# Kernel optimization log

Hardware: AMD Instinct MI355X
Metric: run time of the kernel (lower is better)

The kernel has to match this reference:

```python
import jax, jax.numpy as jnp
import numpy as np
import math

B, L, N, DIM, H = 2, 8, 1024, 512, 8
DH = DIM // H

def setup_inputs() -> dict:
    key = jax.random.key(0)
    ks = jax.random.split(key, 9)
    s = 1.0 / math.sqrt(DIM)
    return {
        "x": jax.random.normal(ks[0], (B, L, N, DIM), dtype=jnp.float32),
        "Wq": jax.random.normal(ks[1], (DIM, DIM), dtype=jnp.float32) * s,
        "bq": jnp.zeros((DIM,), dtype=jnp.float32),
        "Wk": jax.random.normal(ks[2], (DIM, DIM), dtype=jnp.float32) * s,
        "bk": jnp.zeros((DIM,), dtype=jnp.float32),
        "Wv": jax.random.normal(ks[3], (DIM, DIM), dtype=jnp.float32) * s,
        "bv": jnp.zeros((DIM,), dtype=jnp.float32),
        "Wo": jax.random.normal(ks[4], (DIM, DIM), dtype=jnp.float32) * s,
        "bo": jnp.zeros((DIM,), dtype=jnp.float32),
    }

def _split_heads(t):
    # 'b l n (h d) -> b l h n d'
    b, l, n, _ = t.shape
    return t.reshape(b, l, n, H, DH).transpose(0, 1, 3, 2, 4)

def reference(x, Wq, bq, Wk, bk, Wv, bv, Wo, bo):
    q = _split_heads(x @ Wq.T + bq)
    # FAITHFUL BUG: source maps (q, v, k) -> (q_mat, k_mat, v_mat),
    # so the "keys" come from the v projection and "values" from the k projection.
    k_mat = _split_heads(x @ Wv.T + bv)
    v_mat = _split_heads(x @ Wk.T + bk)
    # scale is sqrt(Dh * num_heads) = sqrt(dim), as in the source
    scores = jnp.einsum('blhnd,blhmd->blhnm', q, k_mat) / math.sqrt(DIM)
    weights = jax.nn.softmax(scores, axis=-1)
    inter = jnp.einsum('blhnm,blhmd->blhnd', weights, v_mat)
    # 'b l h n d -> b l n (h d)'
    inter = inter.transpose(0, 1, 3, 2, 4).reshape(x.shape[0], x.shape[1], x.shape[2], DIM)
    return inter @ Wo.T + bo
```

## Files before the change

### kernel.cpp

```cpp
#include <hip/hip_runtime.h>
#include <stdint.h>

#define DIMC 512
#define NSEQ 1024
#define BLT  16
#define NHEAD 8
#define DHD  64
#define MTOT (BLT*NSEQ)
#define LDSW 72
#define PLW  68

typedef float f32x4 __attribute__((ext_vector_type(4)));
typedef short s16x8 __attribute__((ext_vector_type(8)));

__device__ __forceinline__ unsigned short f2bf(float f) {
    unsigned int u = __float_as_uint(f);
    u += 0x7fffu + ((u >> 16) & 1u);
    return (unsigned short)(u >> 16);
}
__device__ __forceinline__ float bf2f(unsigned short h) {
    return __uint_as_float(((unsigned int)h) << 16);
}

#define QSCALE (0.04419417382415922f * 1.4426950408889634f)

__device__ __forceinline__ void gll16(const void* g, void* l) {
    __builtin_amdgcn_global_load_lds(
        (const __attribute__((address_space(1))) void*)g,
        (__attribute__((address_space(3))) void*)l, 16, 0, 0);
}

__global__ void detect_kernel(const unsigned short* __restrict__ x,
                              int* __restrict__ flag) {
    int t = threadIdx.x;
    unsigned short v = x[2 * t];
    int e = (v >> 7) & 0xFF;
    int crazy = (e < 100 || e > 137) ? 1 : 0;
    unsigned long long ball = __ballot(crazy);
    if (t == 0) flag[0] = (__popcll(ball) >= 16) ? 0 : 1;
}

struct ConvArgs {
    const void* src[9];
    unsigned short* dst[9];
};

__global__ __launch_bounds__(256) void conv_kernel(ConvArgs a, const int* __restrict__ flagp) {
    const bool isbf = (*flagp != 0);
    int b = blockIdx.x;
    int seg, idx;
    if (b < 4096)      { seg = 0; idx = (b * 256 + threadIdx.x) * 8; }
    else if (b < 4608) { int t = b - 4096; seg = 1 + (t >> 7);
                         idx = (((t & 127) * 256) + threadIdx.x) * 8; }
    else               { int i = threadIdx.x * 8; seg = 5 + (i >> 9); idx = i & 511; }
    const void* s = a.src[seg];
    unsigned short* d = a.dst[seg];
    if (isbf) {
        *(uint4*)(d + idx) = *(const uint4*)((const unsigned short*)s + idx);
    } else {
        float4 t0 = *(const float4*)((const float*)s + idx);
        float4 t1 = *(const float4*)((const float*)s + idx + 4);
        ushort4 v0{f2bf(t0.x), f2bf(t0.y), f2bf(t0.z), f2bf(t0.w)};
        ushort4 v1{f2bf(t1.x), f2bf(t1.y), f2bf(t1.z), f2bf(t1.w)};
        *(ushort4*)(d + idx)     = v0;
        *(ushort4*)(d + idx + 4) = v1;
    }
}

__device__ __forceinline__ void gemm_core_async(
    const unsigned short* __restrict__ Ap, const unsigned short* __restrict__ Wp,
    int mBase, int nBase, unsigned short* Al, unsigned short* Bl, f32x4 acc[4][4])
{
    const int wave = threadIdx.x >> 6;
    const int lane = threadIdx.x & 63;
    const int lr = lane & 15, lg = lane >> 4;
    const int wm = wave >> 1, wn = wave & 1;
    const int srow = lane >> 3;
    const int scol = (lane & 7) * 8;

    #pragma unroll
    for (int a = 0; a < 4; ++a)
        #pragma unroll
        for (int b = 0; b < 4; ++b) acc[a][b] = (f32x4){0.f, 0.f, 0.f, 0.f};

    for (int k0 = 0; k0 < DIMC; k0 += 64) {
        #pragma unroll
        for (int i = 0; i < 4; ++i) {
            int rbase = (wave * 4 + i) * 8;
            gll16(Ap + (long)(mBase + rbase + srow) * DIMC + k0 + scol, Al + rbase * 64);
            gll16(Wp + (long)(nBase + rbase + srow) * DIMC + k0 + scol, Bl + rbase * 64);
        }
        __syncthreads();

        #pragma unroll
        for (int kk = 0; kk < 64; kk += 32) {
            s16x8 af[4], bf_[4];
            #pragma unroll
            for (int a = 0; a < 4; ++a)
                af[a] = *(const s16x8*)&Al[(wm * 64 + a * 16 + lr) * 64 + kk + lg * 8];
            #pragma unroll
            for (int b = 0; b < 4; ++b)
                bf_[b] = *(const s16x8*)&Bl[(wn * 64 + b * 16 + lr) * 64 + kk + lg * 8];
            #pragma unroll
            for (int a = 0; a < 4; ++a)
                #pragma unroll
                for (int b = 0; b < 4; ++b)
                    acc[a][b] = __builtin_amdgcn_mfma_f32_16x16x32_bf16(af[a], bf_[b], acc[a][b], 0, 0, 0);
        }
        __syncthreads();
    }
}

__global__ __launch_bounds__(256) void proj_kernel(
    const unsigned short* __restrict__ xb,
    const unsigned short* __restrict__ Wqb, const unsigned short* __restrict__ Wkb,
    const unsigned short* __restrict__ Wvb,
    const unsigned short* __restrict__ bqb, const unsigned short* __restrict__ bkb,
    const unsigned short* __restrict__ bvb,
    unsigned short* __restrict__ Q, unsigned short* __restrict__ K,
    unsigned short* __restrict__ Vt)
{
    const int z = blockIdx.z;
    const unsigned short* Wp = (z == 0) ? Wqb : ((z == 1) ? Wvb : Wkb);
    const unsigned short* bp = (z == 0) ? bqb : ((z == 1) ? bvb : bkb);
    unsigned short* outp = (z == 0) ? Q : ((z == 1) ? K : Vt);
    const float oscale = (z == 0) ? QSCALE : 1.0f;

    const int mBase = blockIdx.x * 128;
    const int nBase = blockIdx.y * 128;
    const int lane = threadIdx.x & 63;
    const int lr = lane & 15, lg = lane >> 4;
    const int wm = (threadIdx.x >> 6) >> 1, wn = (threadIdx.x >> 6) & 1;

    __shared__ unsigned short Al[128 * 64];
    __shared__ unsigned short Bl[128 * 64];
    f32x4 acc[4][4];
    gemm_core_async(xb, Wp, mBase, nBase, Al, Bl, acc);

    #pragma unroll
    for (int b = 0; b < 4; ++b) {
        int j = nBase + wn * 64 + b * 16 + lr;
        float bb = bf2f(bp[j]);
        int h = j >> 6, d = j & 63;
        #pragma unroll
        for (int a = 0; a < 4; ++a) {
            int m0 = mBase + wm * 64 + a * 16 + lg * 4;
            int bl = m0 >> 10, n0 = m0 & 1023;
            if (z == 2) {
                ushort4 pk;
                unsigned short* p = (unsigned short*)&pk;
                #pragma unroll
                for (int r = 0; r < 4; ++r) p[r] = f2bf(acc[a][b][r] + bb);
                *(ushort4*)&outp[(((bl << 3) + h) << 16) + (d << 10) + n0] = pk;
            } else {
                #pragma unroll
                for (int r = 0; r < 4; ++r) {
                    float v = (acc[a][b][r] + bb) * oscale;
                    outp[(((bl << 3) + h) << 16) + ((n0 + r) << 6) + d] = f2bf(v);
                }
            }
        }
    }
}

__global__ __launch_bounds__(256) void out_gemm_kernel(
    const unsigned short* __restrict__ inter, const unsigned short* __restrict__ Wob,
    const unsigned short* __restrict__ bob, void* __restrict__ outp,
    const int* __restrict__ flagp)
{
    const bool isbf = (*flagp != 0);
    const int mBase = blockIdx.x * 128;
    const int nBase = blockIdx.y * 128;
    const int lane = threadIdx.x & 63;
    const int lr = lane & 15, lg = lane >> 4;
    const int wm = (threadIdx.x >> 6) >> 1, wn = (threadIdx.x >> 6) & 1;

    __shared__ unsigned short Al[128 * 64];
    __shared__ unsigned short Bl[128 * 64];
    f32x4 acc[4][4];
    gemm_core_async(inter, Wob, mBase, nBase, Al, Bl, acc);

    #pragma unroll
    for (int b = 0; b < 4; ++b) {
        int j = nBase + wn * 64 + b * 16 + lr;
        float bb = bf2f(bob[j]);
        #pragma unroll
        for (int a = 0; a < 4; ++a) {
            #pragma unroll
            for (int r = 0; r < 4; ++r) {
                long m = mBase + wm * 64 + a * 16 + lg * 4 + r;
                float v = acc[a][b][r] + bb;
                if (isbf) ((unsigned short*)outp)[m * DIMC + j] = f2bf(v);
                else      ((float*)outp)[m * DIMC + j] = v;
            }
        }
    }
}

__global__ __launch_bounds__(256) void attn_kernel(
    const unsigned short* __restrict__ Q, const unsigned short* __restrict__ K,
    const unsigned short* __restrict__ Vt, unsigned short* __restrict__ inter)
{
    const int inst = blockIdx.x;
    const int bh = inst >> 4;
    const int qt = inst & 15;
    const int wave = threadIdx.x >> 6;
    const int lane = threadIdx.x & 63;
    const int lr = lane & 15;
    const int lg = lane >> 4;

    const unsigned short* Qb = Q + (long)bh * (NSEQ * DHD);
    const int qrow = qt * 64 + wave * 16 + lr;
    s16x8 qf0 = *(const s16x8*)&Qb[qrow * DHD + lg * 8];
    s16x8 qf1 = *(const s16x8*)&Qb[qrow * DHD + 32 + lg * 8];

    __shared__ unsigned short Kl[64 * LDSW];
    __shared__ unsigned short Vl[64 * LDSW];
    __shared__ unsigned short Pl[4][16 * PLW];

    f32x4 o[4];
    #pragma unroll
    for (int c = 0; c < 4; ++c) o[c] = (f32x4){0.f, 0.f, 0.f, 0.f};
    float l_part[4] = {0.f, 0.f, 0.f, 0.f};

    for (int kt = 0; kt < 16; ++kt) {
        const unsigned short* Kb = K + (long)bh * (NSEQ * DHD) + kt * 64 * DHD;
        const unsigned short* Vb = Vt + (long)bh * (NSEQ * DHD) + kt * 64;

        #pragma unroll
        for (int i = 0; i < 2; ++i) {
            int f = threadIdx.x + 256 * i;
            int row = f >> 3, c8 = (f & 7) * 8;
            *(uint4*)&Kl[row * LDSW + c8] = *(const uint4*)&Kb[row * DHD + c8];
            *(uint4*)&Vl[row * LDSW + c8] = *(const uint4*)&Vb[row * NSEQ + c8];
        }
        __syncthreads();

        f32x4 s[4];
        #pragma unroll
        for (int c = 0; c < 4; ++c) s[c] = (f32x4){0.f, 0.f, 0.f, 0.f};
        #pragma unroll
        for (int kk = 0; kk < 2; ++kk) {
            s16x8 a = kk ? qf1 : qf0;
            #pragma unroll
            for (int c = 0; c < 4; ++c) {
                s16x8 b = *(const s16x8*)&Kl[(c * 16 + lr) * LDSW + kk * 32 + lg * 8];
                s[c] = __builtin_amdgcn_mfma_f32_16x16x32_bf16(a, b, s[c], 0, 0, 0);
            }
        }

        #pragma unroll
        for (int c = 0; c < 4; ++c)
            #pragma unroll
            for (int r = 0; r < 4; ++r) {
                float p = __builtin_exp2f(s[c][r]);
                l_part[r] += p;
                Pl[wave][(lg * 4 + r) * PLW + c * 16 + lr] = f2bf(p);
            }

        #pragma unroll
        for (int kk = 0; kk < 2; ++kk) {
            s16x8 a = *(const s16x8*)&Pl[wave][lr * PLW + kk * 32 + lg * 8];
            #pragma unroll
            for (int c = 0; c < 4; ++c) {
                s16x8 b = *(const s16x8*)&Vl[(c * 16 + lr) * LDSW + kk * 32 + lg * 8];
                o[c] = __builtin_amdgcn_mfma_f32_16x16x32_bf16(a, b, o[c], 0, 0, 0);
            }
        }
        __syncthreads();
    }

    #pragma unroll
    for (int r = 0; r < 4; ++r) {
        #pragma unroll
        for (int msk = 1; msk < 16; msk <<= 1)
            l_part[r] += __shfl_xor(l_part[r], msk);
    }
    const int bl = bh >> 3, h = bh & 7;
    #pragma unroll
    for (int r = 0; r < 4; ++r) {
        float inv = 1.f / l_part[r];
        int n = qt * 64 + wave * 16 + lg * 4 + r;
        #pragma unroll
        for (int c = 0; c < 4; ++c) {
            int col = h * 64 + c * 16 + lr;
            inter[((long)(bl * NSEQ + n)) * DIMC + col] = f2bf(o[c][r] * inv);
        }
    }
}

extern "C" void kernel_launch(void* const* d_in, const int* in_sizes, int n_in,
                              void* d_out, int out_size, void* d_ws, size_t ws_size,
                              hipStream_t stream) {
    const void* x  = d_in[0];
    const void* Wq = d_in[1]; const void* bq = d_in[2];
    const void* Wk = d_in[3]; const void* bk = d_in[4];
    const void* Wv = d_in[5]; const void* bv = d_in[6];
    const void* Wo = d_in[7]; const void* bo = d_in[8];

    char* ws = (char*)d_ws;
    int* flag = (int*)ws;
    unsigned short* xb  = (unsigned short*)(ws + 256);
    unsigned short* Q   = xb + (long)MTOT * DIMC;
    unsigned short* K   = Q  + (long)MTOT * DIMC;
    unsigned short* Vt  = K  + (long)MTOT * DIMC;
    unsigned short* Wqb = Vt + (long)MTOT * DIMC;
    unsigned short* Wkb = Wqb + DIMC * DIMC;
    unsigned short* Wvb = Wkb + DIMC * DIMC;
    unsigned short* Wob = Wvb + DIMC * DIMC;
    unsigned short* bqb = Wob + DIMC * DIMC;
    unsigned short* bkb = bqb + DIMC;
    unsigned short* bvb = bkb + DIMC;
    unsigned short* bob = bvb + DIMC;

    detect_kernel<<<1, 64, 0, stream>>>((const unsigned short*)x, flag);

    ConvArgs ca;
    ca.src[0] = x;  ca.src[1] = Wq; ca.src[2] = Wk; ca.src[3] = Wv; ca.src[4] = Wo;
    ca.src[5] = bq; ca.src[6] = bk; ca.src[7] = bv; ca.src[8] = bo;
    ca.dst[0] = xb;  ca.dst[1] = Wqb; ca.dst[2] = Wkb; ca.dst[3] = Wvb; ca.dst[4] = Wob;
    ca.dst[5] = bqb; ca.dst[6] = bkb; ca.dst[7] = bvb; ca.dst[8] = bob;
    conv_kernel<<<4609, 256, 0, stream>>>(ca, flag);

    dim3 gp(MTOT / 128, DIMC / 128, 3);
    proj_kernel<<<gp, 256, 0, stream>>>(xb, Wqb, Wkb, Wvb, bqb, bkb, bvb, Q, K, Vt);

    attn_kernel<<<BLT * NHEAD * 16, 256, 0, stream>>>(Q, K, Vt, xb );

    dim3 go(MTOT / 128, DIMC / 128);
    out_gemm_kernel<<<go, 256, 0, stream>>>(xb , Wob, bob, d_out, flag);
}
```

Measured before the change: 252.9 us.

## Keep attention probabilities in registers via transposed MFMA and swizzle LDS

Measured after the change: 248.4 us. No clear change (-1.8%).

```diff
diff --git a/kernel.cpp b/kernel.cpp
--- a/kernel.cpp
+++ b/kernel.cpp
@@ -7,11 +7,10 @@
 #define NHEAD 8
 #define DHD  64
 #define MTOT (BLT*NSEQ)
-#define LDSW 72
-#define PLW  68
 
 typedef float f32x4 __attribute__((ext_vector_type(4)));
 typedef short s16x8 __attribute__((ext_vector_type(8)));
+typedef short s16x4 __attribute__((ext_vector_type(4)));
 
 __device__ __forceinline__ unsigned short f2bf(float f) {
     unsigned int u = __float_as_uint(f);
@@ -30,14 +29,22 @@
         (__attribute__((address_space(3))) void*)l, 16, 0, 0);
 }
 
-__global__ void detect_kernel(const unsigned short* __restrict__ x,
-                              int* __restrict__ flag) {
-    int t = threadIdx.x;
+__device__ __forceinline__ f32x4 mfma16_bf16(s16x4 a, s16x4 b, f32x4 c) {
+#if __has_builtin(__builtin_amdgcn_mfma_f32_16x16x16bf16_1k)
+    return __builtin_amdgcn_mfma_f32_16x16x16bf16_1k(a, b, c, 0, 0, 0);
+#else
+    asm volatile("v_mfma_f32_16x16x16_bf16 %0, %1, %2, %0"
+                 : "+v"(c) : "v"(a), "v"(b));
+    return c;
+#endif
+}
+
+__device__ __forceinline__ bool detect_bf16(const unsigned short* x) {
+    int t = threadIdx.x & 63;
     unsigned short v = x[2 * t];
     int e = (v >> 7) & 0xFF;
-    int crazy = (e < 100 || e > 137) ? 1 : 0;
-    unsigned long long ball = __ballot(crazy);
-    if (t == 0) flag[0] = (__popcll(ball) >= 16) ? 0 : 1;
+    unsigned long long ball = __ballot(e < 100 || e > 137);
+    return __popcll(ball) < 16;
 }
 
 struct ConvArgs {
@@ -45,8 +52,9 @@
     unsigned short* dst[9];
 };
 
-__global__ __launch_bounds__(256) void conv_kernel(ConvArgs a, const int* __restrict__ flagp) {
-    const bool isbf = (*flagp != 0);
+__global__ __launch_bounds__(256) void conv_kernel(ConvArgs a,
+                                                   const unsigned short* __restrict__ xdet) {
+    const bool isbf = detect_bf16(xdet);
     int b = blockIdx.x;
     int seg, idx;
     if (b < 4096)      { seg = 0; idx = (b * 256 + threadIdx.x) * 8; }
@@ -166,9 +174,9 @@
 __global__ __launch_bounds__(256) void out_gemm_kernel(
     const unsigned short* __restrict__ inter, const unsigned short* __restrict__ Wob,
     const unsigned short* __restrict__ bob, void* __restrict__ outp,
-    const int* __restrict__ flagp)
+    const unsigned short* __restrict__ xdet)
 {
-    const bool isbf = (*flagp != 0);
+    const bool isbf = detect_bf16(xdet);
     const int mBase = blockIdx.x * 128;
     const int nBase = blockIdx.y * 128;
     const int lane = threadIdx.x & 63;
@@ -196,6 +204,8 @@
         }
     }
 }
+
+#define SWZ(row, col) ((row) * 64 + ((col) ^ (((row) & 7) * 8)))
 
 __global__ __launch_bounds__(256) void attn_kernel(
     const unsigned short* __restrict__ Q, const unsigned short* __restrict__ K,
@@ -214,14 +224,13 @@
     s16x8 qf0 = *(const s16x8*)&Qb[qrow * DHD + lg * 8];
     s16x8 qf1 = *(const s16x8*)&Qb[qrow * DHD + 32 + lg * 8];
 
-    __shared__ unsigned short Kl[64 * LDSW];
-    __shared__ unsigned short Vl[64 * LDSW];
-    __shared__ unsigned short Pl[4][16 * PLW];
+    __shared__ unsigned short Kl[64 * 64];
+    __shared__ unsigned short Vl[64 * 64];
 
     f32x4 o[4];
     #pragma unroll
-    for (int c = 0; c < 4; ++c) o[c] = (f32x4){0.f, 0.f, 0.f, 0.f};
-    float l_part[4] = {0.f, 0.f, 0.f, 0.f};
+    for (int m = 0; m < 4; ++m) o[m] = (f32x4){0.f, 0.f, 0.f, 0.f};
+    float l_acc = 0.f;
 
     for (int kt = 0; kt < 16; ++kt) {
         const unsigned short* Kb = K + (long)bh * (NSEQ * DHD) + kt * 64 * DHD;
@@ -231,8 +240,8 @@
         for (int i = 0; i < 2; ++i) {
             int f = threadIdx.x + 256 * i;
             int row = f >> 3, c8 = (f & 7) * 8;
-            *(uint4*)&Kl[row * LDSW + c8] = *(const uint4*)&Kb[row * DHD + c8];
-            *(uint4*)&Vl[row * LDSW + c8] = *(const uint4*)&Vb[row * NSEQ + c8];
+            *(uint4*)&Kl[SWZ(row, c8)] = *(const uint4*)&Kb[row * DHD + c8];
+            *(uint4*)&Vl[SWZ(row, c8)] = *(const uint4*)&Vb[row * NSEQ + c8];
         }
         __syncthreads();
 
@@ -241,51 +250,55 @@
         for (int c = 0; c < 4; ++c) s[c] = (f32x4){0.f, 0.f, 0.f, 0.f};
         #pragma unroll
         for (int kk = 0; kk < 2; ++kk) {
-            s16x8 a = kk ? qf1 : qf0;
+            s16x8 qf = kk ? qf1 : qf0;
             #pragma unroll
             for (int c = 0; c < 4; ++c) {
-                s16x8 b = *(const s16x8*)&Kl[(c * 16 + lr) * LDSW + kk * 32 + lg * 8];
-                s[c] = __builtin_amdgcn_mfma_f32_16x16x32_bf16(a, b, s[c], 0, 0, 0);
+                s16x8 a = *(const s16x8*)&Kl[SWZ(c * 16 + lr, kk * 32 + lg * 8)];
+                s[c] = __builtin_amdgcn_mfma_f32_16x16x32_bf16(a, qf, s[c], 0, 0, 0);
             }
         }
 
+        s16x4 pb[4];
+        #pragma unroll
+        for (int c = 0; c < 4; ++c) {
+            float p0 = __builtin_exp2f(s[c][0]);
+            float p1 = __builtin_exp2f(s[c][1]);
+            float p2 = __builtin_exp2f(s[c][2]);
+            float p3 = __builtin_exp2f(s[c][3]);
+            l_acc += (p0 + p1) + (p2 + p3);
+            unsigned int u0 = __float_as_uint(p0) + 0x8000u;
+            unsigned int u1 = __float_as_uint(p1) + 0x8000u;
+            unsigned int u2 = __float_as_uint(p2) + 0x8000u;
+            unsigned int u3 = __float_as_uint(p3) + 0x8000u;
+            union { s16x4 v; unsigned int u[2]; } pk;
+            pk.u[0] = __builtin_amdgcn_perm(u1, u0, 0x07060302u);
+            pk.u[1] = __builtin_amdgcn_perm(u3, u2, 0x07060302u);
+            pb[c] = pk.v;
+        }
+
         #pragma unroll
         for (int c = 0; c < 4; ++c)
             #pragma unroll
-            for (int r = 0; r < 4; ++r) {
-                float p = __builtin_exp2f(s[c][r]);
-                l_part[r] += p;
-                Pl[wave][(lg * 4 + r) * PLW + c * 16 + lr] = f2bf(p);
+            for (int m = 0; m < 4; ++m) {
+                s16x4 a = *(const s16x4*)&Vl[SWZ(m * 16 + lr, c * 16 + lg * 4)];
+                o[m] = mfma16_bf16(a, pb[c], o[m]);
             }
-
-        #pragma unroll
-        for (int kk = 0; kk < 2; ++kk) {
-            s16x8 a = *(const s16x8*)&Pl[wave][lr * PLW + kk * 32 + lg * 8];
-            #pragma unroll
-            for (int c = 0; c < 4; ++c) {
-                s16x8 b = *(const s16x8*)&Vl[(c * 16 + lr) * LDSW + kk * 32 + lg * 8];
-                o[c] = __builtin_amdgcn_mfma_f32_16x16x32_bf16(a, b, o[c], 0, 0, 0);
-            }
-        }
         __syncthreads();
     }
 
-    #pragma unroll
-    for (int r = 0; r < 4; ++r) {
-        #pragma unroll
-        for (int msk = 1; msk < 16; msk <<= 1)
-            l_part[r] += __shfl_xor(l_part[r], msk);
-    }
+    l_acc += __shfl_xor(l_acc, 16);
+    l_acc += __shfl_xor(l_acc, 32);
+    float inv = 1.f / l_acc;
+
     const int bl = bh >> 3, h = bh & 7;
-    #pragma unroll
-    for (int r = 0; r < 4; ++r) {
-        float inv = 1.f / l_part[r];
-        int n = qt * 64 + wave * 16 + lg * 4 + r;
-        #pragma unroll
-        for (int c = 0; c < 4; ++c) {
-            int col = h * 64 + c * 16 + lr;
-            inter[((long)(bl * NSEQ + n)) * DIMC + col] = f2bf(o[c][r] * inv);
-        }
+    const int n = qt * 64 + wave * 16 + lr;
+    #pragma unroll
+    for (int m = 0; m < 4; ++m) {
+        ushort4 pk;
+        unsigned short* p = (unsigned short*)&pk;
+        #pragma unroll
+        for (int r = 0; r < 4; ++r) p[r] = f2bf(o[m][r] * inv);
+        *(ushort4*)&inter[((long)(bl * NSEQ + n)) * DIMC + h * 64 + m * 16 + lg * 4] = pk;
     }
 }
 
@@ -299,8 +312,7 @@
     const void* Wo = d_in[7]; const void* bo = d_in[8];
 
     char* ws = (char*)d_ws;
-    int* flag = (int*)ws;
-    unsigned short* xb  = (unsigned short*)(ws + 256);
+    unsigned short* xb  = (unsigned short*)ws;
     unsigned short* Q   = xb + (long)MTOT * DIMC;
     unsigned short* K   = Q  + (long)MTOT * DIMC;
     unsigned short* Vt  = K  + (long)MTOT * DIMC;
@@ -313,14 +325,12 @@
     unsigned short* bvb = bkb + DIMC;
     unsigned short* bob = bvb + DIMC;
 
-    detect_kernel<<<1, 64, 0, stream>>>((const unsigned short*)x, flag);
-
     ConvArgs ca;
     ca.src[0] = x;  ca.src[1] = Wq; ca.src[2] = Wk; ca.src[3] = Wv; ca.src[4] = Wo;
     ca.src[5] = bq; ca.src[6] = bk; ca.src[7] = bv; ca.src[8] = bo;
     ca.dst[0] = xb;  ca.dst[1] = Wqb; ca.dst[2] = Wkb; ca.dst[3] = Wvb; ca.dst[4] = Wob;
     ca.dst[5] = bqb; ca.dst[6] = bkb; ca.dst[7] = bvb; ca.dst[8] = bob;
-    conv_kernel<<<4609, 256, 0, stream>>>(ca, flag);
+    conv_kernel<<<4609, 256, 0, stream>>>(ca, (const unsigned short*)x);
 
     dim3 gp(MTOT / 128, DIMC / 128, 3);
     proj_kernel<<<gp, 256, 0, stream>>>(xb, Wqb, Wkb, Wvb, bqb, bkb, bvb, Q, K, Vt);
@@ -328,5 +338,6 @@
     attn_kernel<<<BLT * NHEAD * 16, 256, 0, stream>>>(Q, K, Vt, xb );
 
     dim3 go(MTOT / 128, DIMC / 128);
-    out_gemm_kernel<<<go, 256, 0, stream>>>(xb , Wob, bob, d_out, flag);
-}
+    out_gemm_kernel<<<go, 256, 0, stream>>>(xb , Wob, bob, d_out,
+                                            (const unsigned short*)x);
+}
```
